# Optimization experiments

Hardware: AMD Instinct MI355X
Metric: run time of the kernel (lower is better)

## Reference

```python
import jax, jax.numpy as jnp
import numpy as np

CHUNK = 32      # args.chunk_size
MEM = 64        # args.mem_size (fixed-capacity steady state)
EPS = 1e-10


def setup_inputs() -> dict:
    key = jax.random.key(0)
    k1, k2 = jax.random.split(key)
    x = jax.random.normal(k1, (16, 4096, 512), dtype=jnp.float32)
    mem_init = jax.random.normal(k2, (16, 64, 512), dtype=jnp.float32)
    return {"x": x, "mem_init": mem_init}


def _memory_bank_update(x, mem_init):
    B, T, D = x.shape
    C, M = CHUNK, MEM
    n_chunks = T // C
    xc = x[:, : n_chunks * C].reshape(B, n_chunks, C, D).transpose(1, 0, 2, 3)  # [n,B,C,D]
    inv_sqrt_d = 1.0 / jnp.sqrt(jnp.asarray(D, x.dtype))
    # threshold = 0.5 * log2(mem_size) as in the source
    threshold = 0.5 * jnp.log2(jnp.asarray(M, x.dtype) + EPS)

    def step(carry, chunk):  # chunk: [B, C, D]
        mem, m_score, m_freq = carry
        # cross-attention score of chunk tokens over memory slots
        logits = jnp.einsum('bcd,bmd->bcm', chunk, mem) * inv_sqrt_d
        score = jax.nn.softmax(logits, axis=-1).mean(axis=1)          # [B, M]
        new_m = chunk.max(axis=1)                                      # maxpool over chunk -> [B, D]
        entropy = (-jnp.log2(score + EPS) * score).sum(axis=1).mean()  # scalar (mean over batch)

        # --- path 1 (entropy > threshold): score-based slot replacement ---
        ms1 = m_score + score
        mf1 = m_freq + 1.0
        repl = jnp.argmin(ms1 / mf1, axis=1)                           # lowest avg-score slot, [B]
        oh1 = jax.nn.one_hot(repl, M, dtype=mem.dtype)                 # [B, M]
        mem1 = mem * (1.0 - oh1[..., None]) + oh1[..., None] * new_m[:, None, :]
        ms1 = ms1 * (1.0 - oh1)          # fresh slot starts with zero score
        mf1 = mf1 * (1.0 - oh1) + oh1    # and freq 1

        # --- path 2 (entropy <= threshold): cosine-sim nearest-slot merge ---
        nmn = new_m / jnp.sqrt((new_m * new_m).sum(-1, keepdims=True) + 1e-8)
        mn = mem / jnp.sqrt((mem * mem).sum(-1, keepdims=True) + 1e-8)
        sim = jnp.einsum('bd,bmd->bm', nmn, mn)                        # [B, M]
        idx = jnp.argmax(sim, axis=1)
        oh2 = jax.nn.one_hot(idx, M, dtype=mem.dtype)
        # mem[b,idx] += 0.7*new_m - 0.7*mem[b,idx]  ->  0.3*old + 0.7*new
        mem2 = mem + oh2[..., None] * (0.7 * new_m[:, None, :] - 0.7 * mem)

        take1 = entropy > threshold
        mem_n = jnp.where(take1, mem1, mem2)
        ms_n = jnp.where(take1, ms1, m_score)
        mf_n = jnp.where(take1, mf1, m_freq)
        return (mem_n, ms_n, mf_n), score

    init = (mem_init,
            jnp.zeros((B, M), x.dtype),
            jnp.zeros((B, M), x.dtype))
    (mem, m_score, m_freq), _ = jax.lax.scan(step, init, xc)
    return mem  # [B, M, D]


def reference(x, mem_init):
    return _memory_bank_update(x, mem_init)
```

## Files before the change

### kernel.cpp

```cpp
#include <hip/hip_runtime.h>
#include <stdint.h>

#define NB 16
#define TT 4096
#define DD 512
#define CC 32
#define MM 64
#define NCH 128
#define NSRC 192
#define ROWW 36
#define TOTROWS 16320
#define KS 32

#define WS_NEWM 0
#define WS_NN2  (NB*NCH*DD)
#define WS_GX   (WS_NN2 + NB*NCH)
#define WS_CTL  (WS_GX + (size_t)NB*TOTROWS*ROWW)

__device__ __forceinline__ float wredsum(float v){
#pragma unroll
  for (int o = 32; o > 0; o >>= 1) v += __shfl_xor(v, o);
  return v;
}
__device__ __forceinline__ float wredmax(float v){
#pragma unroll
  for (int o = 32; o > 0; o >>= 1) v = fmaxf(v, __shfl_xor(v, o));
  return v;
}

__global__ __launch_bounds__(256)
void k1_newm(const float* __restrict__ x, float* __restrict__ ws)
{
  __shared__ float part[4];
  const int bid = blockIdx.x;
  const int b = bid >> 7, t = bid & 127;
  const int tid = threadIdx.x;
  const float* xb = x + ((size_t)b*TT + (size_t)t*CC)*DD;
  const int k0 = tid*2;
  float v0 = -INFINITY, v1 = -INFINITY;
#pragma unroll
  for (int c = 0; c < CC; ++c){
    const float2 xv = *(const float2*)(xb + (size_t)c*DD + k0);
    v0 = fmaxf(v0, xv.x); v1 = fmaxf(v1, xv.y);
  }
  float* nm = ws + WS_NEWM + ((size_t)b*NCH + t)*DD;
  nm[k0] = v0; nm[k0+1] = v1;
  float p = wredsum(v0*v0 + v1*v1);
  if ((tid & 63) == 0) part[tid >> 6] = p;
  __syncthreads();
  if (tid == 0) ws[WS_NN2 + (size_t)b*NCH + t] = part[0]+part[1]+part[2]+part[3];
}

__global__ __launch_bounds__(512)
void k2_gemm(const float* __restrict__ x, const float* __restrict__ mem_init,
             float* __restrict__ ws)
{
  __shared__ float Xs[KS][128];
  __shared__ float Ss[KS][NSRC];

  const int b  = blockIdx.x;
  const int tg = blockIdx.y;
  const int tid = threadIdx.x;
  const int rowlim = min(NSRC, 68 + 4*tg);
  const int T0 = tg*128;

  const int ot = tid & 15;
  const int rs = tid >> 4;
  const bool active = (rs*6 < rowlim);

  float acc[6][8];
#pragma unroll
  for (int j = 0; j < 6; ++j)
#pragma unroll
    for (int i = 0; i < 8; ++i) acc[j][i] = 0.0f;

  const float* xb    = x + ((size_t)b*TT + T0)*DD;
  const float* nmarr = ws + WS_NEWM + (size_t)b*NCH*DD;

  const int xtok = tid >> 2;
  const int xkq  = tid & 3;
  const int srow = tid >> 1;
  const int shalf= tid & 1;
  const float* srcrow = nullptr;
  if (tid < 384 && srow < rowlim)
    srcrow = (srow < MM) ? (mem_init + ((size_t)b*MM + srow)*DD)
                         : (nmarr + (size_t)(srow - MM)*DD);

  for (int ks = 0; ks < DD/KS; ++ks){
    const int k0 = ks*KS;
    {
      const float* p = xb + (size_t)xtok*DD + k0 + xkq*8;
      const float4 a  = *(const float4*)p;
      const float4 c4 = *(const float4*)(p + 4);
      const int kb = xkq*8;
      Xs[kb+0][xtok]=a.x;  Xs[kb+1][xtok]=a.y;  Xs[kb+2][xtok]=a.z;  Xs[kb+3][xtok]=a.w;
      Xs[kb+4][xtok]=c4.x; Xs[kb+5][xtok]=c4.y; Xs[kb+6][xtok]=c4.z; Xs[kb+7][xtok]=c4.w;
    }
    if (srcrow){
      const float* p = srcrow + k0 + shalf*16;
#pragma unroll
      for (int q = 0; q < 4; ++q){
        const float4 a = *(const float4*)(p + q*4);
        const int kb = shalf*16 + q*4;
        Ss[kb+0][srow]=a.x; Ss[kb+1][srow]=a.y; Ss[kb+2][srow]=a.z; Ss[kb+3][srow]=a.w;
      }
    }
    __syncthreads();
    if (active){
#pragma unroll
      for (int k = 0; k < KS; ++k){
        const float4 x0 = *(const float4*)&Xs[k][ot*8];
        const float4 x1 = *(const float4*)&Xs[k][ot*8 + 4];
        const float2 r0 = *(const float2*)&Ss[k][rs*6];
        const float2 r1 = *(const float2*)&Ss[k][rs*6 + 2];
        const float2 r2 = *(const float2*)&Ss[k][rs*6 + 4];
        const float xv[8] = {x0.x,x0.y,x0.z,x0.w,x1.x,x1.y,x1.z,x1.w};
        const float rv[6] = {r0.x,r0.y,r1.x,r1.y,r2.x,r2.y};
#pragma unroll
        for (int j = 0; j < 6; ++j)
#pragma unroll
          for (int i = 0; i < 8; ++i)
            acc[j][i] = fmaf(rv[j], xv[i], acc[j][i]);
      }
    }
    __syncthreads();
  }

  const float inv_sqrt_d = 1.0f / sqrtf((float)DD);
  const int t  = tg*4 + (ot >> 2);
  const int c0 = (ot & 3)*8;
  float* gbase = ws + WS_GX + ((size_t)b*TOTROWS + (size_t)(64*t + (t*(t-1))/2))*ROWW;
#pragma unroll
  for (int j = 0; j < 6; ++j){
    const int row = rs*6 + j;
    if (row < 64 + t){
      float* g = gbase + (size_t)row*ROWW + c0;
      float4 o0 = {acc[j][0]*inv_sqrt_d, acc[j][1]*inv_sqrt_d,
                   acc[j][2]*inv_sqrt_d, acc[j][3]*inv_sqrt_d};
      float4 o1 = {acc[j][4]*inv_sqrt_d, acc[j][5]*inv_sqrt_d,
                   acc[j][6]*inv_sqrt_d, acc[j][7]*inv_sqrt_d};
      *(float4*)g = o0;
      *(float4*)(g + 4) = o1;
    }
  }
}

__global__ __launch_bounds__(256)
void k2_nn(const float* __restrict__ mem_init, float* __restrict__ ws)
{
  __shared__ float nm[DD];
  const int b = blockIdx.x, t = blockIdx.y;
  const int tid = threadIdx.x, lane = tid & 63, w = tid >> 6;
  const float* nmarr = ws + WS_NEWM + (size_t)b*NCH*DD;
  {
    const float2 v = *(const float2*)(nmarr + (size_t)t*DD + tid*2);
    nm[tid*2] = v.x; nm[tid*2+1] = v.y;
  }
  __syncthreads();
  const float4 na = *(const float4*)(nm + lane*8);
  const float4 nc = *(const float4*)(nm + lane*8 + 4);
  const int nrows = MM + t;
  float* gbase = ws + WS_GX + ((size_t)b*TOTROWS + (size_t)(64*t + (t*(t-1))/2))*ROWW;
  for (int r = w; r < nrows; r += 4){
    const float* src = (r < MM) ? (mem_init + ((size_t)b*MM + r)*DD)
                                : (nmarr + (size_t)(r - MM)*DD);
    const float4 a  = *(const float4*)(src + lane*8);
    const float4 c4 = *(const float4*)(src + lane*8 + 4);
    float d = a.x*na.x + a.y*na.y + a.z*na.z + a.w*na.w
            + c4.x*nc.x + c4.y*nc.y + c4.z*nc.z + c4.w*nc.w;
    d = wredsum(d);
    if (lane == 0) gbase[(size_t)r*ROWW + 32] = d;
  }
}

__global__ __launch_bounds__(1024)
void k3_scan(const float* __restrict__ mem_init, float* __restrict__ ws,
             float* __restrict__ out)
{
  __shared__ float Llds[CC][65];
  __shared__ float Elds[CC][65];
  __shared__ float P1[16][65];
  __shared__ float P2[16][65];
  __shared__ float dense[MM][NSRC];
  __shared__ float S_base[CC], Mx[CC], E1c[CC], E2c[CC], R1[CC], R2[CC];
  __shared__ float s_sc[MM], s_fr[MM], s_n2[MM];
  __shared__ float s_sdB[MM];
  __shared__ float s_sdCur[MM];
  __shared__ float s_scoreP[MM], s_scoreC[MM];
  __shared__ int   s_srcRow[MM], s_isC[MM];
  __shared__ float s_rnmNN, s_sd1v, s_sd2v, s_n2v1, s_n2v2;
  __shared__ int   s_d, s_i1p, s_i2p, s_oldC2, s_oldR2;

  const int tid  = threadIdx.x;
  const int lane = tid & 63;
  const int w    = tid >> 6;
  const int b    = blockIdx.x;
  const int wu   = __builtin_amdgcn_readfirstlane(w);

  const float* newmarr = ws + WS_NEWM;
  const float* nn2arr  = ws + WS_NN2;
  const float* gx      = ws + WS_GX;
  unsigned long long* ctl = (unsigned long long*)(ws + WS_CTL);

  const int  gm  = tid >> 4;
  const int  gc2 = (tid & 15)*2;
  const bool gl  = ((tid & 15) == 0);

  if (tid < MM){ s_sc[tid]=0.f; s_fr[tid]=0.f; s_srcRow[tid]=tid; s_isC[tid]=0; }
#pragma unroll
  for (int it = 0; it < 4; ++it){
    const int m0 = wu + it*16;
    const float* src = mem_init + ((size_t)b*MM + m0)*DD;
    const float4 a  = *(const float4*)(src + lane*8);
    const float4 c4 = *(const float4*)(src + lane*8 + 4);
    float p = a.x*a.x + a.y*a.y + a.z*a.z + a.w*a.w
            + c4.x*c4.x + c4.y*c4.y + c4.z*c4.z + c4.w*c4.w;
    p = wredsum(p);
    if (lane == 0) s_n2[m0] = p;
  }
  __syncthreads();

  {
    const float* gx0 = gx + (size_t)b*TOTROWS*ROWW;
    const float* grow = gx0 + (size_t)gm*ROWW;
    const float2 p = *(const float2*)(grow + gc2);
    Llds[gc2][gm] = p.x; Llds[gc2+1][gm] = p.y;
    if (gl) s_sdCur[gm] = grow[32];
  }
  __syncthreads();
  {
#pragma unroll
    for (int rr = 0; rr < 2; ++rr){
      const int c = 2*wu + rr;
      const float l = Llds[c][lane];
      const float mx = wredmax(l);
      const float e = expf(l - mx);
      const float S = wredsum(e);
      Elds[c][lane] = e;
      if (lane == 0){ S_base[c] = S; Mx[c] = mx; }
    }
  }
  __syncthreads();
  {
    const int m = tid & 63, g = tid >> 6;
    const int c0 = 2*g, c1 = c0 + 1;
    P1[g][m] = Elds[c0][m]/S_base[c0] + Elds[c1][m]/S_base[c1];
  }
  __syncthreads();
  if (wu == 0){
    float s0 = 0.f;
#pragma unroll
    for (int g = 0; g < 16; ++g) s0 += P1[g][lane];
    s0 *= 0.03125f;
    s_scoreC[lane] = s0;
    const float ent0 = wredsum(-log2f(s0 + 1e-10f) * s0);
    if (lane == 0){
      const unsigned long long v = ((unsigned long long)1u << 32)
                                 | (unsigned long long)__float_as_uint(ent0);
      __hip_atomic_store(&ctl[b], v, __ATOMIC_RELEASE, __HIP_MEMORY_SCOPE_AGENT);
    }
  }
  __syncthreads();

  for (int t = 0; t < NCH; ++t){
    const float nn2_t = nn2arr[(size_t)b*NCH + t];

    if (t > 0){
      const int d = s_d;
      const int m1 = s_i1p, m2 = s_i2p;
      if (d){
        if (tid < MM){
          float ns = s_sc[tid] + s_scoreP[tid];
          float nf = s_fr[tid] + 1.0f;
          if (tid == m1){ ns = 0.0f; nf = 1.0f; }
          s_sc[tid] = ns; s_fr[tid] = nf;
          s_sdCur[tid] = (tid == m1) ? s_sd1v : s_sdB[tid];
        }
        if (tid == 512){
          s_srcRow[m1] = 64 + (t-1);
          s_isC[m1] = 0;
          s_n2[m1] = s_n2v1;
        }
      } else {
        if (tid < NSRC){
          float val = s_oldC2 ? 0.3f*dense[m2][tid] : ((tid == s_oldR2) ? 0.3f : 0.0f);
          if (tid == 64 + (t-1)) val += 0.7f;
          dense[m2][tid] = val;
        }
        if (tid < MM) s_sdCur[tid] = (tid == m2) ? s_sd2v : s_sdB[tid];
        if (tid == 512){
          s_isC[m2] = 1;
          s_n2[m2] = s_n2v2;
        }
      }
    }
    __syncthreads();

    if (t < NCH-1){
      const float* gxn = gx + ((size_t)b*TOTROWS
                         + (size_t)(64*(t+1) + ((t+1)*t)/2))*ROWW;
      float v0, v1, sd = 0.f;
      if (!s_isC[gm]){
        const float* grow = gxn + (size_t)s_srcRow[gm]*ROWW;
        const float2 p = *(const float2*)(grow + gc2);
        v0 = p.x; v1 = p.y;
        if (gl) sd = grow[32];
      } else {
        v0 = 0.f; v1 = 0.f;
        const int ns = 65 + t;
        for (int s2 = 0; s2 < ns; ++s2){
          const float co = dense[gm][s2];
          if (co != 0.0f){
            const float* grow = gxn + (size_t)s2*ROWW;
            v0 = fmaf(co, grow[gc2],   v0);
            v1 = fmaf(co, grow[gc2+1], v1);
            if (gl) sd = fmaf(co, grow[32], sd);
          }
        }
      }
      Llds[gc2][gm] = v0; Llds[gc2+1][gm] = v1;
      if (gl) s_sdB[gm] = sd;
      if (tid < 32) {
        Llds[tid][64] = gxn[(size_t)(64+t)*ROWW + tid];
      }
      if (tid == 32) s_rnmNN = gxn[(size_t)(64+t)*ROWW + 32];
    }
    __syncthreads();

    if (wu == 0){
      float q = (s_sc[lane] + s_scoreC[lane]) / (s_fr[lane] + 1.0f);
      int idx = lane;
#pragma unroll
      for (int o = 32; o > 0; o >>= 1){
        const float ov = __shfl_xor(q, o);
        const int   oi = __shfl_xor(idx, o);
        if (ov < q || (ov == q && oi < idx)){ q = ov; idx = oi; }
      }
      if (lane == 0) s_i1p = idx;
      if (t < NCH-1){
#pragma unroll
        for (int rr = 0; rr < 2; ++rr){
          const int c = 28 + rr;
          const float l = Llds[c][lane];
          const float mx = wredmax(l);
          const float e = expf(l - mx);
          const float S = wredsum(e);
          Elds[c][lane] = e;
          if (lane == 0){ S_base[c] = S; Mx[c] = mx; }
        }
      }
    } else if (wu == 1){
      float sim = s_sdCur[lane] / (sqrtf(nn2_t + 1e-8f) * sqrtf(s_n2[lane] + 1e-8f));
      int idx = lane;
#pragma unroll
      for (int o = 32; o > 0; o >>= 1){
        const float ov = __shfl_xor(sim, o);
        const int   oi = __shfl_xor(idx, o);
        if (ov > sim || (ov == sim && oi < idx)){ sim = ov; idx = oi; }
      }
      if (lane == 0){
        s_i2p = idx;
        s_oldC2 = s_isC[idx];
        s_oldR2 = s_srcRow[idx];
        s_n2v2 = 0.09f*s_n2[idx] + 0.42f*s_sdCur[idx] + 0.49f*nn2_t;
        s_n2v1 = nn2_t;
      }
      if (t < NCH-1){
#pragma unroll
        for (int rr = 0; rr < 2; ++rr){
          const int c = 30 + rr;
          const float l = Llds[c][lane];
          const float mx = wredmax(l);
          const float e = expf(l - mx);
          const float S = wredsum(e);
          Elds[c][lane] = e;
          if (lane == 0){ S_base[c] = S; Mx[c] = mx; }
        }
      }
    } else {
      if (t < NCH-1){
#pragma unroll
        for (int rr = 0; rr < 2; ++rr){
          const int c = 2*(wu-2) + rr;
          const float l = Llds[c][lane];
          const float mx = wredmax(l);
          const float e = expf(l - mx);
          const float S = wredsum(e);
          Elds[c][lane] = e;
          if (lane == 0){ S_base[c] = S; Mx[c] = mx; }
        }
      }
    }
    __syncthreads();

    if (t < NCH-1){
      if (wu == 0 && lane < 32){
        const int c = lane;
        const int m1 = s_i1p;
        const float e1 = expf(Llds[c][64] - Mx[c]);
        const float S1 = S_base[c] - Elds[c][m1] + e1;
        E1c[c] = e1; R1[c] = 1.0f / S1;
        if (c == 0) s_sd1v = s_rnmNN;
      } else if (wu == 1 && lane < 32){
        const int c = lane;
        const int m2 = s_i2p;
        const float l2 = 0.3f*Llds[c][m2] + 0.7f*Llds[c][64];
        const float e2 = expf(l2 - Mx[c]);
        const float S2 = S_base[c] - Elds[c][m2] + e2;
        E2c[c] = e2; R2[c] = 1.0f / S2;
        if (c == 0) s_sd2v = 0.3f*s_sdB[m2] + 0.7f*s_rnmNN;
      }
    }
    __syncthreads();

    if (t < NCH-1){
      const int m = tid & 63, g = tid >> 6;
      const int c0 = 2*g, c1 = c0 + 1;
      const int m1 = s_i1p, m2 = s_i2p;
      const float ea0 = Elds[c0][m], ea1 = Elds[c1][m];
      const float p1 = ((m==m1)?E1c[c0]:ea0)*R1[c0] + ((m==m1)?E1c[c1]:ea1)*R1[c1];
      const float p2 = ((m==m2)?E2c[c0]:ea0)*R2[c0] + ((m==m2)?E2c[c1]:ea1)*R2[c1];
      P1[g][m] = p1;
      P2[g][m] = p2;
    }
    __syncthreads();

    if (wu == 0){
      float s1 = 0.f, s2 = 0.f, ent1 = 0.f, ent2 = 0.f;
      if (t < NCH-1){
#pragma unroll
        for (int g = 0; g < 16; ++g){ s1 += P1[g][lane]; s2 += P2[g][lane]; }
        s1 *= 0.03125f; s2 *= 0.03125f;
        ent1 = wredsum(-log2f(s1 + 1e-10f) * s1);
        ent2 = wredsum(-log2f(s2 + 1e-10f) * s2);
      }
      float ev = 0.f;
      if (lane < NB){
        unsigned long long vv;
        do {
          vv = __hip_atomic_load(&ctl[(t&1)*16 + lane], __ATOMIC_ACQUIRE,
                                 __HIP_MEMORY_SCOPE_AGENT);
        } while ((unsigned)(vv >> 32) != (unsigned)(t+1));
        ev = __uint_as_float((unsigned)vv);
      }
      const float tot = wredsum(ev);
      const int d = (tot * (1.0f/16.0f) > 3.0f) ? 1 : 0;
      if (t < NCH-1){
        if (lane == 0){
          const float entp = d ? ent1 : ent2;
          const unsigned long long v = ((unsigned long long)(unsigned)(t+2) << 32)
                                     | (unsigned long long)__float_as_uint(entp);
          __hip_atomic_store(&ctl[((t+1)&1)*16 + b], v, __ATOMIC_RELEASE,
                             __HIP_MEMORY_SCOPE_AGENT);
        }
        s_scoreP[lane] = s_scoreC[lane];
        s_scoreC[lane] = d ? s1 : s2;
      }
      if (lane == 0) s_d = d;
    }
    __syncthreads();
  }

  {
    const int d = s_d;
    if (d){
      if (tid == 0){ s_srcRow[s_i1p] = 64 + (NCH-1); s_isC[s_i1p] = 0; }
    } else {
      const int i = s_i2p;
      if (tid < NSRC){
        float val = s_oldC2 ? 0.3f*dense[i][tid] : ((tid == s_oldR2) ? 0.3f : 0.0f);
        if (tid == 64 + (NCH-1)) val += 0.7f;
        dense[i][tid] = val;
      }
      if (tid == 0) s_isC[i] = 1;
    }
  }
  __syncthreads();

#pragma unroll
  for (int it = 0; it < 4; ++it){
    const int mo = wu + it*16;
    const int k0 = lane*8;
    float o8[8];
    if (!s_isC[mo]){
      const int row = s_srcRow[mo];
      const float* vec = (row < MM) ? (mem_init + ((size_t)b*MM + row)*DD)
                                    : (newmarr + ((size_t)b*NCH + (row - MM))*DD);
#pragma unroll
      for (int j = 0; j < 8; ++j) o8[j] = vec[k0 + j];
    } else {
#pragma unroll
      for (int j = 0; j < 8; ++j) o8[j] = 0.0f;
      for (int s = 0; s < NSRC; ++s){
        const float co = dense[mo][s];
        if (co != 0.0f){
          const float* vec = (s < MM) ? (mem_init + ((size_t)b*MM + s)*DD)
                                      : (newmarr + ((size_t)b*NCH + (s - MM))*DD);
#pragma unroll
          for (int j = 0; j < 8; ++j) o8[j] = fmaf(co, vec[k0 + j], o8[j]);
        }
      }
    }
    float* dst = out + ((size_t)b*MM + mo)*DD + k0;
#pragma unroll
    for (int j = 0; j < 8; ++j) dst[j] = o8[j];
  }
}

extern "C" void kernel_launch(void* const* d_in, const int* in_sizes, int n_in,
                              void* d_out, int out_size, void* d_ws, size_t ws_size,
                              hipStream_t stream)
{
  const float* x  = (const float*)d_in[0];
  const float* mi = (const float*)d_in[1];
  float* out = (float*)d_out;
  float* ws  = (float*)d_ws;
  hipLaunchKernelGGL(k1_newm, dim3(NB*NCH), dim3(256), 0, stream, x, ws);
  hipLaunchKernelGGL(k2_gemm, dim3(NB, 32), dim3(512), 0, stream, x, mi, ws);
  hipLaunchKernelGGL(k2_nn,   dim3(NB, NCH), dim3(256), 0, stream, mi, ws);
  hipLaunchKernelGGL(k3_scan, dim3(NB), dim3(1024), 0, stream, mi, ws, out);
}
```

Before: 943.5 us.

## Fuse new-mem dot products into GEMM, merge scan phases, pad control flags

Folds the k2_nn kernel into k2_gemm: four threads per row-slice also accumulate dot products of each chunk's pooled vector against the source rows already staged in shared memory, which removes one launch and its reread of global memory. In the scan kernel, the per-chunk exp/reciprocal phase is merged into the probability phase, with each wave recomputing its own values, so one block barrier per step goes away. The cross-block control flags are spread to 64-byte spacing and switched to relaxed atomics to cut false sharing and fence cost. Relaxed ordering could weaken the visibility guarantees of the inter-block handshake.

```diff
diff --git a/kernel.cpp b/kernel.cpp
--- a/kernel.cpp
+++ b/kernel.cpp
@@ -67,12 +67,14 @@
   const int ot = tid & 15;
   const int rs = tid >> 4;
   const bool active = (rs*6 < rowlim);
+  const bool nnact  = (ot < 4);
 
   float acc[6][8];
 #pragma unroll
   for (int j = 0; j < 6; ++j)
 #pragma unroll
     for (int i = 0; i < 8; ++i) acc[j][i] = 0.0f;
+  float nnacc[6] = {0,0,0,0,0,0};
 
   const float* xb    = x + ((size_t)b*TT + T0)*DD;
   const float* nmarr = ws + WS_NEWM + (size_t)b*NCH*DD;
@@ -107,6 +109,7 @@
     }
     __syncthreads();
     if (active){
+      const int nrow = 64 + tg*4 + ot;
 #pragma unroll
       for (int k = 0; k < KS; ++k){
         const float4 x0 = *(const float4*)&Xs[k][ot*8];
@@ -121,6 +124,12 @@
 #pragma unroll
           for (int i = 0; i < 8; ++i)
             acc[j][i] = fmaf(rv[j], xv[i], acc[j][i]);
+        if (nnact){
+          const float nv = Ss[k][nrow];
+#pragma unroll
+          for (int j = 0; j < 6; ++j)
+            nnacc[j] = fmaf(nv, rv[j], nnacc[j]);
+        }
       }
     }
     __syncthreads();
@@ -143,33 +152,14 @@
       *(float4*)(g + 4) = o1;
     }
   }
-}
-
-__global__ __launch_bounds__(256)
-void k2_nn(const float* __restrict__ mem_init, float* __restrict__ ws)
-{
-  __shared__ float nm[DD];
-  const int b = blockIdx.x, t = blockIdx.y;
-  const int tid = threadIdx.x, lane = tid & 63, w = tid >> 6;
-  const float* nmarr = ws + WS_NEWM + (size_t)b*NCH*DD;
-  {
-    const float2 v = *(const float2*)(nmarr + (size_t)t*DD + tid*2);
-    nm[tid*2] = v.x; nm[tid*2+1] = v.y;
-  }
-  __syncthreads();
-  const float4 na = *(const float4*)(nm + lane*8);
-  const float4 nc = *(const float4*)(nm + lane*8 + 4);
-  const int nrows = MM + t;
-  float* gbase = ws + WS_GX + ((size_t)b*TOTROWS + (size_t)(64*t + (t*(t-1))/2))*ROWW;
-  for (int r = w; r < nrows; r += 4){
-    const float* src = (r < MM) ? (mem_init + ((size_t)b*MM + r)*DD)
-                                : (nmarr + (size_t)(r - MM)*DD);
-    const float4 a  = *(const float4*)(src + lane*8);
-    const float4 c4 = *(const float4*)(src + lane*8 + 4);
-    float d = a.x*na.x + a.y*na.y + a.z*na.z + a.w*na.w
-            + c4.x*nc.x + c4.y*nc.y + c4.z*nc.z + c4.w*nc.w;
-    d = wredsum(d);
-    if (lane == 0) gbase[(size_t)r*ROWW + 32] = d;
+  if (nnact){
+    const int tn = tg*4 + ot;
+    float* gb = ws + WS_GX + ((size_t)b*TOTROWS + (size_t)(64*tn + (tn*(tn-1))/2))*ROWW;
+#pragma unroll
+    for (int j = 0; j < 6; ++j){
+      const int row = rs*6 + j;
+      if (row < 64 + tn) gb[(size_t)row*ROWW + 32] = nnacc[j];
+    }
   }
 }
 
@@ -182,7 +172,7 @@
   __shared__ float P1[16][65];
   __shared__ float P2[16][65];
   __shared__ float dense[MM][NSRC];
-  __shared__ float S_base[CC], Mx[CC], E1c[CC], E2c[CC], R1[CC], R2[CC];
+  __shared__ float S_base[CC], Mx[CC];
   __shared__ float s_sc[MM], s_fr[MM], s_n2[MM];
   __shared__ float s_sdB[MM];
   __shared__ float s_sdCur[MM];
@@ -257,7 +247,7 @@
     if (lane == 0){
       const unsigned long long v = ((unsigned long long)1u << 32)
                                  | (unsigned long long)__float_as_uint(ent0);
-      __hip_atomic_store(&ctl[b], v, __ATOMIC_RELEASE, __HIP_MEMORY_SCOPE_AGENT);
+      __hip_atomic_store(&ctl[b*8], v, __ATOMIC_RELAXED, __HIP_MEMORY_SCOPE_AGENT);
     }
   }
   __syncthreads();
@@ -320,9 +310,8 @@
       }
       Llds[gc2][gm] = v0; Llds[gc2+1][gm] = v1;
       if (gl) s_sdB[gm] = sd;
-      if (tid < 32) {
+      if (tid < 32)
         Llds[tid][64] = gxn[(size_t)(64+t)*ROWW + tid];
-      }
       if (tid == 32) s_rnmNN = gxn[(size_t)(64+t)*ROWW + 32];
     }
     __syncthreads();
@@ -394,34 +383,26 @@
     __syncthreads();
 
     if (t < NCH-1){
-      if (wu == 0 && lane < 32){
-        const int c = lane;
-        const int m1 = s_i1p;
-        const float e1 = expf(Llds[c][64] - Mx[c]);
-        const float S1 = S_base[c] - Elds[c][m1] + e1;
-        E1c[c] = e1; R1[c] = 1.0f / S1;
-        if (c == 0) s_sd1v = s_rnmNN;
-      } else if (wu == 1 && lane < 32){
-        const int c = lane;
-        const int m2 = s_i2p;
-        const float l2 = 0.3f*Llds[c][m2] + 0.7f*Llds[c][64];
-        const float e2 = expf(l2 - Mx[c]);
-        const float S2 = S_base[c] - Elds[c][m2] + e2;
-        E2c[c] = e2; R2[c] = 1.0f / S2;
-        if (c == 0) s_sd2v = 0.3f*s_sdB[m2] + 0.7f*s_rnmNN;
-      }
-    }
-    __syncthreads();
-
-    if (t < NCH-1){
-      const int m = tid & 63, g = tid >> 6;
+      const int m = lane, g = wu;
       const int c0 = 2*g, c1 = c0 + 1;
       const int m1 = s_i1p, m2 = s_i2p;
+      const float e1c0 = expf(Llds[c0][64] - Mx[c0]);
+      const float e1c1 = expf(Llds[c1][64] - Mx[c1]);
+      const float r1c0 = 1.0f / (S_base[c0] - Elds[c0][m1] + e1c0);
+      const float r1c1 = 1.0f / (S_base[c1] - Elds[c1][m1] + e1c1);
+      const float l2c0 = 0.3f*Llds[c0][m2] + 0.7f*Llds[c0][64];
+      const float l2c1 = 0.3f*Llds[c1][m2] + 0.7f*Llds[c1][64];
+      const float e2c0 = expf(l2c0 - Mx[c0]);
+      const float e2c1 = expf(l2c1 - Mx[c1]);
+      const float r2c0 = 1.0f / (S_base[c0] - Elds[c0][m2] + e2c0);
+      const float r2c1 = 1.0f / (S_base[c1] - Elds[c1][m2] + e2c1);
       const float ea0 = Elds[c0][m], ea1 = Elds[c1][m];
-      const float p1 = ((m==m1)?E1c[c0]:ea0)*R1[c0] + ((m==m1)?E1c[c1]:ea1)*R1[c1];
-      const float p2 = ((m==m2)?E2c[c0]:ea0)*R2[c0] + ((m==m2)?E2c[c1]:ea1)*R2[c1];
-      P1[g][m] = p1;
-      P2[g][m] = p2;
+      P1[g][m] = ((m==m1)?e1c0:ea0)*r1c0 + ((m==m1)?e1c1:ea1)*r1c1;
+      P2[g][m] = ((m==m2)?e2c0:ea0)*r2c0 + ((m==m2)?e2c1:ea1)*r2c1;
+      if (wu == 2 && lane == 0){
+        s_sd1v = s_rnmNN;
+        s_sd2v = 0.3f*s_sdB[m2] + 0.7f*s_rnmNN;
+      }
     }
     __syncthreads();
 
@@ -438,7 +419,7 @@
       if (lane < NB){
         unsigned long long vv;
         do {
-          vv = __hip_atomic_load(&ctl[(t&1)*16 + lane], __ATOMIC_ACQUIRE,
+          vv = __hip_atomic_load(&ctl[((t&1)*16 + lane)*8], __ATOMIC_RELAXED,
                                  __HIP_MEMORY_SCOPE_AGENT);
         } while ((unsigned)(vv >> 32) != (unsigned)(t+1));
         ev = __uint_as_float((unsigned)vv);
@@ -450,7 +431,7 @@
           const float entp = d ? ent1 : ent2;
           const unsigned long long v = ((unsigned long long)(unsigned)(t+2) << 32)
                                      | (unsigned long long)__float_as_uint(entp);
-          __hip_atomic_store(&ctl[((t+1)&1)*16 + b], v, __ATOMIC_RELEASE,
+          __hip_atomic_store(&ctl[(((t+1)&1)*16 + b)*8], v, __ATOMIC_RELAXED,
                              __HIP_MEMORY_SCOPE_AGENT);
         }
         s_scoreP[lane] = s_scoreC[lane];
@@ -517,6 +498,5 @@
   float* ws  = (float*)d_ws;
   hipLaunchKernelGGL(k1_newm, dim3(NB*NCH), dim3(256), 0, stream, x, ws);
   hipLaunchKernelGGL(k2_gemm, dim3(NB, 32), dim3(512), 0, stream, x, mi, ws);
-  hipLaunchKernelGGL(k2_nn,   dim3(NB, NCH), dim3(256), 0, stream, mi, ws);
   hipLaunchKernelGGL(k3_scan, dim3(NB), dim3(1024), 0, stream, mi, ws, out);
 }
```

After: 2.492 ms. 164% more time.
